# Kernel optimization log

Measured on AMD Instinct MI355X. Metric: run time of the kernel, lower is better.

## Reference

```python
import jax, jax.numpy as jnp
import numpy as np

B, TE, TD, H = 8, 512, 128, 256

def setup_inputs() -> dict:
    key = jax.random.key(0)
    k1, k2, k3, k4, k5 = jax.random.split(key, 5)
    return {
        "encoder_outputs": jax.random.normal(k1, (B, TE, H), dtype=jnp.float32),
        "decoder_outputs": jax.random.normal(k2, (B, TD, H), dtype=jnp.float32),
        "W_a": jax.random.normal(k3, (H, H), dtype=jnp.float32) * (1.0 / np.sqrt(H)),
        "U_a": jax.random.normal(k4, (H, H), dtype=jnp.float32) * (1.0 / np.sqrt(H)),
        "V_a": jax.random.normal(k5, (H, 1), dtype=jnp.float32) * (1.0 / np.sqrt(H)),
    }

def reference(encoder_outputs, decoder_outputs, W_a, U_a, V_a):
    # Bahdanau additive attention.
    enc_proj = jnp.einsum("beh,hk->bek", encoder_outputs, W_a)   # [B,TE,H]
    dec_proj = jnp.einsum("bdh,hk->bdk", decoder_outputs, U_a)   # [B,TD,H]
    # Broadcast add -> tanh -> project with V_a: [B,TD,TE]
    score = jnp.tanh(enc_proj[:, None, :, :] + dec_proj[:, :, None, :])  # [B,TD,TE,H]
    score = jnp.einsum("bdeh,h->bde", score, V_a[:, 0])          # [B,TD,TE]
    attention_weights = jax.nn.softmax(score, axis=-1)           # over encoder positions
    context = jnp.einsum("bde,beh->bdh", attention_weights, encoder_outputs)
    return (context, attention_weights)
```

## Files before the change

kernel.cpp:

```cpp
#include <hip/hip_runtime.h>
#include <hip/hip_bf16.h>

#ifndef __has_builtin
#define __has_builtin(x) 0
#endif

constexpr int B_ = 8, TE_ = 512, TD_ = 128, H_ = 256;
constexpr float TWO_LOG2E = 2.8853900817779268f;
constexpr float LOG2E = 1.4426950408889634f;

typedef float  vf2    __attribute__((ext_vector_type(2)));
typedef short  bf16x8 __attribute__((ext_vector_type(8)));
typedef float  f32x4  __attribute__((ext_vector_type(4)));

__device__ __forceinline__ float exp2_fast(float x) {
#if __has_builtin(__builtin_amdgcn_exp2f)
  return __builtin_amdgcn_exp2f(x);
#else
  return exp2f(x);
#endif
}
__device__ __forceinline__ float rcp_fast(float x) {
#if __has_builtin(__builtin_amdgcn_rcpf)
  return __builtin_amdgcn_rcpf(x);
#else
  return 1.0f / x;
#endif
}
__device__ __forceinline__ vf2 fma2(vf2 a, vf2 b, vf2 c) {
#if __has_builtin(__builtin_elementwise_fma)
  return __builtin_elementwise_fma(a, b, c);
#else
  vf2 r; r.x = __fmaf_rn(a.x, b.x, c.x); r.y = __fmaf_rn(a.y, b.y, c.y); return r;
#endif
}
__device__ __forceinline__ void bf16split(float x, unsigned short& hi, unsigned short& lo) {
  unsigned u = __float_as_uint(x);
  hi = (unsigned short)(u >> 16);
  float hif = __uint_as_float((unsigned)hi << 16);
  lo = (unsigned short)(__float_as_uint(x - hif) >> 16);
}

__global__ __launch_bounds__(256)
void proj_mfma(const float* __restrict__ enc, const float* __restrict__ dec,
               const float* __restrict__ W, const float* __restrict__ U,
               float* __restrict__ ep, float* __restrict__ dp) {
  __shared__ unsigned short Ah[32][40], Al[32][40], Bh[32][40], Bl[32][40];
  const int tid = threadIdx.x;
  const int mt = blockIdx.x;
  const int n0 = blockIdx.y * 32;
  const float* A; const float* Bm; float* C; int row0;
  if (mt < 128) { A = enc; Bm = W; C = ep; row0 = mt * 32; }
  else          { A = dec; Bm = U; C = dp; row0 = (mt - 128) * 32; }
  const int w = tid >> 6, lane = tid & 63;
  const int mw = (w & 1) * 16, nw = (w >> 1) * 16;
  const int quad = lane >> 4, l16 = lane & 15;
  const int am = tid >> 3, ak = (tid & 7) * 4;
  const int bn = tid & 31, bk = (tid >> 5) * 4;

  f32x4 acc = {0.f, 0.f, 0.f, 0.f};
  for (int k0 = 0; k0 < H_; k0 += 32) {
    float4 a4 = *(const float4*)&A[(long)(row0 + am) * H_ + k0 + ak];
    unsigned short h0, l0, h1, l1, h2, l2, h3, l3;
    bf16split(a4.x, h0, l0); bf16split(a4.y, h1, l1);
    bf16split(a4.z, h2, l2); bf16split(a4.w, h3, l3);
    *(ushort4*)&Ah[am][ak] = make_ushort4(h0, h1, h2, h3);
    *(ushort4*)&Al[am][ak] = make_ushort4(l0, l1, l2, l3);
    float b0 = Bm[(long)(k0 + bk + 0) * H_ + n0 + bn];
    float b1 = Bm[(long)(k0 + bk + 1) * H_ + n0 + bn];
    float b2 = Bm[(long)(k0 + bk + 2) * H_ + n0 + bn];
    float b3 = Bm[(long)(k0 + bk + 3) * H_ + n0 + bn];
    bf16split(b0, h0, l0); bf16split(b1, h1, l1);
    bf16split(b2, h2, l2); bf16split(b3, h3, l3);
    *(ushort4*)&Bh[bn][bk] = make_ushort4(h0, h1, h2, h3);
    *(ushort4*)&Bl[bn][bk] = make_ushort4(l0, l1, l2, l3);
    __syncthreads();
    bf16x8 ah = *(const bf16x8*)&Ah[mw + l16][quad * 8];
    bf16x8 al = *(const bf16x8*)&Al[mw + l16][quad * 8];
    bf16x8 bh = *(const bf16x8*)&Bh[nw + l16][quad * 8];
    bf16x8 bl = *(const bf16x8*)&Bl[nw + l16][quad * 8];
    acc = __builtin_amdgcn_mfma_f32_16x16x32_bf16(ah, bh, acc, 0, 0, 0);
    acc = __builtin_amdgcn_mfma_f32_16x16x32_bf16(ah, bl, acc, 0, 0, 0);
    acc = __builtin_amdgcn_mfma_f32_16x16x32_bf16(al, bh, acc, 0, 0, 0);
    __syncthreads();
  }
#pragma unroll
  for (int r = 0; r < 4; ++r)
    C[(long)(row0 + mw + quad * 4 + r) * H_ + n0 + nw + l16] = acc[r] * TWO_LOG2E;
}

__global__ __launch_bounds__(256)
void score_kernel(const float* __restrict__ ep, const float* __restrict__ dp,
                  const float* __restrict__ v, float* __restrict__ sc) {
  __shared__ __align__(16) float eps[32][68];
  __shared__ __align__(16) float dps[16][68];
  __shared__ __align__(16) float vs[64];
  const int tid = threadIdx.x;
  const int b = blockIdx.z;
  const int e0 = blockIdx.x * 32;
  const int d0 = blockIdx.y * 16;
  const int e = tid & 31;
  const int dg = tid >> 5;
  vf2 acc0 = {0.f, 0.f}, acc1 = {0.f, 0.f};

  for (int h0 = 0; h0 < H_; h0 += 64) {
#pragma unroll
    for (int i = 0; i < 2; ++i) {
      int idx = tid + i * 256;
      int r = idx >> 4, c = (idx & 15) << 2;
      *(float4*)&eps[r][c] = *(const float4*)&ep[(long)(b * TE_ + e0 + r) * H_ + h0 + c];
    }
    {
      int r = tid >> 4, c = (tid & 15) << 2;
      *(float4*)&dps[r][c] = *(const float4*)&dp[(long)(b * TD_ + d0 + r) * H_ + h0 + c];
    }
    if (tid < 16) {
      float4 v4 = *(const float4*)&v[h0 + tid * 4];
      float4 o; o.x = -2.f * v4.x; o.y = -2.f * v4.y; o.z = -2.f * v4.z; o.w = -2.f * v4.w;
      *(float4*)&vs[tid * 4] = o;
    }
    __syncthreads();
    const vf2 one2 = {1.f, 1.f};
#pragma unroll
    for (int hh = 0; hh < 64; hh += 4) {
      vf2 ev0 = *(const vf2*)&eps[e][hh];
      vf2 ev1 = *(const vf2*)&eps[e][hh + 2];
      vf2 vv0 = *(const vf2*)&vs[hh];
      vf2 vv1 = *(const vf2*)&vs[hh + 2];
      vf2 da0 = *(const vf2*)&dps[dg * 2 + 0][hh];
      vf2 da1 = *(const vf2*)&dps[dg * 2 + 0][hh + 2];
      vf2 db0 = *(const vf2*)&dps[dg * 2 + 1][hh];
      vf2 db1 = *(const vf2*)&dps[dg * 2 + 1][hh + 2];
      vf2 g0 = ev0 + da0, g1 = ev1 + da1;
      vf2 h0 = ev0 + db0, h1 = ev1 + db1;
      vf2 t0, t1, u0, u1;
      t0.x = exp2_fast(g0.x); t0.y = exp2_fast(g0.y);
      t1.x = exp2_fast(g1.x); t1.y = exp2_fast(g1.y);
      u0.x = exp2_fast(h0.x); u0.y = exp2_fast(h0.y);
      u1.x = exp2_fast(h1.x); u1.y = exp2_fast(h1.y);
      t0 = t0 + one2; t1 = t1 + one2; u0 = u0 + one2; u1 = u1 + one2;
      vf2 r0, r1, s0, s1;
      r0.x = rcp_fast(t0.x); r0.y = rcp_fast(t0.y);
      r1.x = rcp_fast(t1.x); r1.y = rcp_fast(t1.y);
      s0.x = rcp_fast(u0.x); s0.y = rcp_fast(u0.y);
      s1.x = rcp_fast(u1.x); s1.y = rcp_fast(u1.y);
      acc0 = fma2(vv0, r0, acc0); acc0 = fma2(vv1, r1, acc0);
      acc1 = fma2(vv0, s0, acc1); acc1 = fma2(vv1, s1, acc1);
    }
    __syncthreads();
  }
  long base = ((long)b * TD_ + d0 + dg * 2) * TE_ + e0 + e;
  sc[base] = acc0.x + acc0.y;
  sc[base + TE_] = acc1.x + acc1.y;
}

__global__ __launch_bounds__(64)
void softmax_kernel(const float* __restrict__ sc, float* __restrict__ attn) {
  const long row = blockIdx.x;
  const float* pin = sc + row * TE_;
  float* pout = attn + row * TE_;
  const int t = threadIdx.x;
  float x[8];
  float m = -1e30f;
#pragma unroll
  for (int k = 0; k < 8; ++k) { x[k] = pin[t + 64 * k]; m = fmaxf(m, x[k]); }
#pragma unroll
  for (int off = 32; off; off >>= 1) m = fmaxf(m, __shfl_xor(m, off, 64));
  float s = 0.f;
#pragma unroll
  for (int k = 0; k < 8; ++k) { x[k] = exp2_fast((x[k] - m) * LOG2E); s += x[k]; }
#pragma unroll
  for (int off = 32; off; off >>= 1) s += __shfl_xor(s, off, 64);
  const float r = rcp_fast(s);
#pragma unroll
  for (int k = 0; k < 8; ++k) pout[t + 64 * k] = x[k] * r;
}

__global__ __launch_bounds__(256)
void ctx_mfma(const float* __restrict__ attn, const float* __restrict__ enc,
              float* __restrict__ ctx) {
  __shared__ unsigned short Ah[32][40], Al[32][40], Bh[32][40], Bl[32][40];
  const int tid = threadIdx.x;
  const int m0 = blockIdx.x * 32;
  const int n0 = blockIdx.y * 32;
  const int b = blockIdx.z;
  const float* A = attn + (long)b * TD_ * TE_;
  const float* E = enc + (long)b * TE_ * H_;
  const int w = tid >> 6, lane = tid & 63;
  const int mw = (w & 1) * 16, nw = (w >> 1) * 16;
  const int quad = lane >> 4, l16 = lane & 15;
  const int am = tid >> 3, ak = (tid & 7) * 4;
  const int bn = tid & 31, bk = (tid >> 5) * 4;

  f32x4 acc = {0.f, 0.f, 0.f, 0.f};
  for (int k0 = 0; k0 < TE_; k0 += 32) {
    float4 a4 = *(const float4*)&A[(long)(m0 + am) * TE_ + k0 + ak];
    unsigned short h0, l0, h1, l1, h2, l2, h3, l3;
    bf16split(a4.x, h0, l0); bf16split(a4.y, h1, l1);
    bf16split(a4.z, h2, l2); bf16split(a4.w, h3, l3);
    *(ushort4*)&Ah[am][ak] = make_ushort4(h0, h1, h2, h3);
    *(ushort4*)&Al[am][ak] = make_ushort4(l0, l1, l2, l3);
    float b0 = E[(long)(k0 + bk + 0) * H_ + n0 + bn];
    float b1 = E[(long)(k0 + bk + 1) * H_ + n0 + bn];
    float b2 = E[(long)(k0 + bk + 2) * H_ + n0 + bn];
    float b3 = E[(long)(k0 + bk + 3) * H_ + n0 + bn];
    bf16split(b0, h0, l0); bf16split(b1, h1, l1);
    bf16split(b2, h2, l2); bf16split(b3, h3, l3);
    *(ushort4*)&Bh[bn][bk] = make_ushort4(h0, h1, h2, h3);
    *(ushort4*)&Bl[bn][bk] = make_ushort4(l0, l1, l2, l3);
    __syncthreads();
    bf16x8 ah = *(const bf16x8*)&Ah[mw + l16][quad * 8];
    bf16x8 al = *(const bf16x8*)&Al[mw + l16][quad * 8];
    bf16x8 bh = *(const bf16x8*)&Bh[nw + l16][quad * 8];
    bf16x8 bl = *(const bf16x8*)&Bl[nw + l16][quad * 8];
    acc = __builtin_amdgcn_mfma_f32_16x16x32_bf16(ah, bh, acc, 0, 0, 0);
    acc = __builtin_amdgcn_mfma_f32_16x16x32_bf16(ah, bl, acc, 0, 0, 0);
    acc = __builtin_amdgcn_mfma_f32_16x16x32_bf16(al, bh, acc, 0, 0, 0);
    __syncthreads();
  }
#pragma unroll
  for (int r = 0; r < 4; ++r)
    ctx[((long)b * TD_ + m0 + mw + quad * 4 + r) * H_ + n0 + nw + l16] = acc[r];
}

extern "C" void kernel_launch(void* const* d_in, const int* in_sizes, int n_in,
                              void* d_out, int out_size, void* d_ws, size_t ws_size,
                              hipStream_t stream) {
  const float* enc = (const float*)d_in[0];
  const float* dec = (const float*)d_in[1];
  const float* Wa  = (const float*)d_in[2];
  const float* Ua  = (const float*)d_in[3];
  const float* Va  = (const float*)d_in[4];

  float* out  = (float*)d_out;
  float* ctx  = out;
  float* attn = out + (long)B_ * TD_ * H_;

  float* ep = (float*)d_ws;
  float* dp = ep + (long)B_ * TE_ * H_;
  float* sc = dp + (long)B_ * TD_ * H_;

  proj_mfma<<<dim3(160, 8), 256, 0, stream>>>(enc, dec, Wa, Ua, ep, dp);
  score_kernel<<<dim3(TE_ / 32, TD_ / 16, B_), 256, 0, stream>>>(ep, dp, Va, sc);
  softmax_kernel<<<dim3(B_ * TD_), 64, 0, stream>>>(sc, attn);
  ctx_mfma<<<dim3(TD_ / 32, H_ / 32, B_), 256, 0, stream>>>(attn, enc, ctx);
}
```

Before: 108.9 us.

## Split score reduction over H into two halves and sum partials in softmax

```diff
diff --git a/kernel.cpp b/kernel.cpp
--- a/kernel.cpp
+++ b/kernel.cpp
@@ -96,14 +96,16 @@
   __shared__ __align__(16) float dps[16][68];
   __shared__ __align__(16) float vs[64];
   const int tid = threadIdx.x;
-  const int b = blockIdx.z;
+  const int bz = blockIdx.z;
+  const int b = bz >> 1;
+  const int h_lo = (bz & 1) * 128;
   const int e0 = blockIdx.x * 32;
   const int d0 = blockIdx.y * 16;
   const int e = tid & 31;
   const int dg = tid >> 5;
   vf2 acc0 = {0.f, 0.f}, acc1 = {0.f, 0.f};
 
-  for (int h0 = 0; h0 < H_; h0 += 64) {
+  for (int h0 = h_lo; h0 < h_lo + 128; h0 += 64) {
 #pragma unroll
     for (int i = 0; i < 2; ++i) {
       int idx = tid + i * 256;
@@ -123,21 +125,21 @@
     const vf2 one2 = {1.f, 1.f};
 #pragma unroll
     for (int hh = 0; hh < 64; hh += 4) {
-      vf2 ev0 = *(const vf2*)&eps[e][hh];
-      vf2 ev1 = *(const vf2*)&eps[e][hh + 2];
-      vf2 vv0 = *(const vf2*)&vs[hh];
-      vf2 vv1 = *(const vf2*)&vs[hh + 2];
-      vf2 da0 = *(const vf2*)&dps[dg * 2 + 0][hh];
-      vf2 da1 = *(const vf2*)&dps[dg * 2 + 0][hh + 2];
-      vf2 db0 = *(const vf2*)&dps[dg * 2 + 1][hh];
-      vf2 db1 = *(const vf2*)&dps[dg * 2 + 1][hh + 2];
+      float4 evf = *(const float4*)&eps[e][hh];
+      float4 vvf = *(const float4*)&vs[hh];
+      float4 daf = *(const float4*)&dps[dg * 2 + 0][hh];
+      float4 dbf = *(const float4*)&dps[dg * 2 + 1][hh];
+      vf2 ev0 = {evf.x, evf.y}, ev1 = {evf.z, evf.w};
+      vf2 vv0 = {vvf.x, vvf.y}, vv1 = {vvf.z, vvf.w};
+      vf2 da0 = {daf.x, daf.y}, da1 = {daf.z, daf.w};
+      vf2 db0 = {dbf.x, dbf.y}, db1 = {dbf.z, dbf.w};
       vf2 g0 = ev0 + da0, g1 = ev1 + da1;
-      vf2 h0 = ev0 + db0, h1 = ev1 + db1;
+      vf2 h0v = ev0 + db0, h1v = ev1 + db1;
       vf2 t0, t1, u0, u1;
       t0.x = exp2_fast(g0.x); t0.y = exp2_fast(g0.y);
       t1.x = exp2_fast(g1.x); t1.y = exp2_fast(g1.y);
-      u0.x = exp2_fast(h0.x); u0.y = exp2_fast(h0.y);
-      u1.x = exp2_fast(h1.x); u1.y = exp2_fast(h1.y);
+      u0.x = exp2_fast(h0v.x); u0.y = exp2_fast(h0v.y);
+      u1.x = exp2_fast(h1v.x); u1.y = exp2_fast(h1v.y);
       t0 = t0 + one2; t1 = t1 + one2; u0 = u0 + one2; u1 = u1 + one2;
       vf2 r0, r1, s0, s1;
       r0.x = rcp_fast(t0.x); r0.y = rcp_fast(t0.y);
@@ -149,7 +151,7 @@
     }
     __syncthreads();
   }
-  long base = ((long)b * TD_ + d0 + dg * 2) * TE_ + e0 + e;
+  long base = ((long)(bz & 1) * B_ * TD_ + (long)b * TD_ + d0 + dg * 2) * TE_ + e0 + e;
   sc[base] = acc0.x + acc0.y;
   sc[base + TE_] = acc1.x + acc1.y;
 }
@@ -157,13 +159,17 @@
 __global__ __launch_bounds__(64)
 void softmax_kernel(const float* __restrict__ sc, float* __restrict__ attn) {
   const long row = blockIdx.x;
-  const float* pin = sc + row * TE_;
+  const float* p0 = sc + row * TE_;
+  const float* p1 = sc + ((long)B_ * TD_ + row) * TE_;
   float* pout = attn + row * TE_;
   const int t = threadIdx.x;
   float x[8];
   float m = -1e30f;
 #pragma unroll
-  for (int k = 0; k < 8; ++k) { x[k] = pin[t + 64 * k]; m = fmaxf(m, x[k]); }
+  for (int k = 0; k < 8; ++k) {
+    x[k] = p0[t + 64 * k] + p1[t + 64 * k];
+    m = fmaxf(m, x[k]);
+  }
 #pragma unroll
   for (int off = 32; off; off >>= 1) m = fmaxf(m, __shfl_xor(m, off, 64));
   float s = 0.f;
@@ -241,7 +247,7 @@
   float* sc = dp + (long)B_ * TD_ * H_;
 
   proj_mfma<<<dim3(160, 8), 256, 0, stream>>>(enc, dec, Wa, Ua, ep, dp);
-  score_kernel<<<dim3(TE_ / 32, TD_ / 16, B_), 256, 0, stream>>>(ep, dp, Va, sc);
+  score_kernel<<<dim3(TE_ / 32, TD_ / 16, 2 * B_), 256, 0, stream>>>(ep, dp, Va, sc);
   softmax_kernel<<<dim3(B_ * TD_), 64, 0, stream>>>(sc, attn);
   ctx_mfma<<<dim3(TD_ / 32, H_ / 32, B_), 256, 0, stream>>>(attn, enc, ctx);
 }
```

New measurement: 109.1 us. Within noise of the previous version (+0.2%).
